# Kernel optimization log

Measured on AMD Instinct MI355X. Metric: run time of the kernel, lower is better.

## Reference

```python
import jax, jax.numpy as jnp
import numpy as np

E = 768   # embed_dim
N = 12    # num_heads
H = 128   # height
W = 128   # width
D = E // N  # head_dim = 64


def setup_inputs() -> dict:
    key = jax.random.key(0)
    ks = jax.random.split(key, 9)
    s = 0.02
    x = jax.random.normal(ks[0], (1, H * W, E), jnp.float32)
    Wq = jax.random.normal(ks[1], (E, E), jnp.float32) * s
    bq = jnp.zeros((E,), jnp.float32)
    Wk = jax.random.normal(ks[2], (E, E), jnp.float32) * s
    bk = jnp.zeros((E,), jnp.float32)
    Wv = jax.random.normal(ks[3], (E, E), jnp.float32) * s
    bv = jnp.zeros((E,), jnp.float32)
    Wo = jax.random.normal(ks[4], (E, E), jnp.float32) * s
    bo = jnp.zeros((E,), jnp.float32)
    return {"x": x, "Wq": Wq, "bq": bq, "Wk": Wk, "bk": bk,
            "Wv": Wv, "bv": bv, "Wo": Wo, "bo": bo}


def reference(x, Wq, bq, Wk, bk, Wv, bv, Wo, bo):
    # projections (torch Linear: x @ W.T + b)
    q = x @ Wq.T + bq
    k = x @ Wk.T + bk
    v = x @ Wv.T + bv

    # q, k -> (1, N, H, W, D)
    q = q.reshape(1, H, W, N, D).transpose(0, 3, 1, 2, 4)
    k = k.reshape(1, H, W, N, D).transpose(0, 3, 1, 2, 4)

    # --- width-axis attention (per row h) ---
    qr_w = q.transpose(0, 2, 1, 3, 4)  # (1, H, N, W, D)
    kr_w = k.transpose(0, 2, 1, 3, 4)  # (1, H, N, W, D)
    v = v.reshape(1, H, W, N, D).transpose(0, 1, 3, 2, 4)  # (1, H, N, W, D)
    # NOTE: original applies no 1/sqrt(D) scaling
    qk_w = jnp.einsum('bhnwd,bhnvd->bhnwv', qr_w, kr_w)  # (1, H, N, W, W)
    qk_w = jax.nn.softmax(qk_w, axis=-1)
    v = jnp.einsum('bhnwv,bhnvd->bhnwd', qk_w, v)  # (1, H, N, W, D)

    # --- height-axis attention (per column w) ---
    qr_h = q.transpose(0, 3, 1, 2, 4)  # (1, W, N, H, D)
    kr_h = k.transpose(0, 3, 1, 2, 4)  # (1, W, N, H, D)
    v = v.transpose(0, 3, 2, 1, 4)     # (1, W, N, H, D)
    qk_h = jnp.einsum('bwnhd,bwngd->bwnhg', qr_h, kr_h)  # (1, W, N, H, H)
    qk_h = jax.nn.softmax(qk_h, axis=-1)
    out = jnp.einsum('bwnhg,bwngd->bwnhd', qk_h, v)  # (1, W, N, H, D)

    # (1, W, N, H, D) -> (1, H, W, N, D) -> (1, H, W, E)
    out = out.transpose(0, 3, 1, 2, 4).reshape(1, H, W, E)
    out = out @ Wo.T + bo
    return out.reshape(1, H * W, E)
```

## Files before the change

kernel.cpp:

```cpp
#include <hip/hip_runtime.h>

typedef __attribute__((ext_vector_type(4))) float f32x4;
typedef __attribute__((ext_vector_type(8))) unsigned short u16x8;
typedef __attribute__((ext_vector_type(8))) __bf16 bf16x8;

typedef __attribute__((address_space(3))) unsigned lds_u32;
typedef const __attribute__((address_space(1))) unsigned glb_u32;

__device__ __forceinline__ unsigned short f2bf(float f) {
    union { float f; unsigned u; } v; v.f = f;
    unsigned r = v.u + 0x7fffu + ((v.u >> 16) & 1u);
    return (unsigned short)(r >> 16);
}

__device__ __forceinline__ f32x4 mfma16(u16x8 a, u16x8 b, f32x4 c) {
    return __builtin_amdgcn_mfma_f32_16x16x32_bf16(
        __builtin_bit_cast(bf16x8, a), __builtin_bit_cast(bf16x8, b), c, 0, 0, 0);
}

__device__ __forceinline__ void gload16(const unsigned short* g, unsigned short* l) {
    __builtin_amdgcn_global_load_lds((glb_u32*)g, (lds_u32*)l, 16, 0, 0);
}

#define BARM() asm volatile("s_barrier" ::: "memory")
#define WAITLGKM0() do { asm volatile("s_waitcnt lgkmcnt(0)" ::: "memory"); \
                         __builtin_amdgcn_sched_barrier(0); } while (0)
#define WAITVM6() asm volatile("s_waitcnt vmcnt(6)" ::: "memory")
#define WAITVM0() asm volatile("s_waitcnt vmcnt(0)" ::: "memory")

__global__ void cvt_f32_bf16(const float* __restrict__ src,
                             unsigned short* __restrict__ dst, int n) {
    int stride = gridDim.x * blockDim.x * 4;
    for (int i = (blockIdx.x * blockDim.x + threadIdx.x) * 4; i < n; i += stride) {
        float4 f = *reinterpret_cast<const float4*>(src + i);
        ushort4 o;
        o.x = f2bf(f.x); o.y = f2bf(f.y); o.z = f2bf(f.z); o.w = f2bf(f.w);
        *reinterpret_cast<ushort4*>(dst + i) = o;
    }
}

__global__ void cvt4_f32_bf16(const float* __restrict__ s0, const float* __restrict__ s1,
                              const float* __restrict__ s2, const float* __restrict__ s3,
                              unsigned short* __restrict__ dst, int per) {
    int total = per * 4;
    int stride = gridDim.x * blockDim.x * 4;
    for (int i = (blockIdx.x * blockDim.x + threadIdx.x) * 4; i < total; i += stride) {
        int w = i / per, off = i - w * per;
        const float* s = w == 0 ? s0 : w == 1 ? s1 : w == 2 ? s2 : s3;
        float4 f = *reinterpret_cast<const float4*>(s + off);
        ushort4 o;
        o.x = f2bf(f.x); o.y = f2bf(f.y); o.z = f2bf(f.z); o.w = f2bf(f.w);
        *reinterpret_cast<ushort4*>(dst + i) = o;
    }
}

template<bool OUTF32>
__global__ __launch_bounds__(512, 2) void gemm256(
    const unsigned short* __restrict__ A,
    const unsigned short* __restrict__ B,
    const float* __restrict__ b0, const float* __restrict__ b1, const float* __restrict__ b2,
    void* __restrict__ C0, void* __restrict__ C1, void* __restrict__ C2,
    int K, int NBY)
{
    __shared__ char lds[131072];
    const int t = threadIdx.x, lane = t & 63, wave = t >> 6;
    const int wm = wave >> 2, wn = wave & 3;

    const int nwg = gridDim.x;
    const int bid = blockIdx.x;
    const int swzb = (bid & 7) * (nwg >> 3) + (bid >> 3);
    const long m0 = (long)(swzb / NBY) * 256;
    const long n0 = (long)(swzb % NBY) * 256;

    const int NT = K >> 6;

    const int rloc = t >> 3;
    const int cel  = ((t & 7) ^ ((t >> 3) & 7)) << 3;
    const unsigned short* Abase = A + (m0 + rloc) * (long)K + cel;
    const unsigned short* Bbase = B + (n0 + rloc) * (long)K + cel;

    auto STAGEA = [&](int kt, int h) {
        char* dst = lds + ((kt & 1) << 15) + (h << 14) + (wave << 10);
        const unsigned short* src = Abase + (long)(h * 128) * K + kt * 64;
        gload16(src, (unsigned short*)dst);
        gload16(src + (long)64 * K, (unsigned short*)(dst + 8192));
    };
    auto STAGEB = [&](int kt, int h) {
        char* dst = lds + 65536 + ((kt & 1) << 15) + (h << 14) + (wave << 10);
        const unsigned short* src = Bbase + (long)(h * 128) * K + kt * 64;
        gload16(src, (unsigned short*)dst);
        gload16(src + (long)64 * K, (unsigned short*)(dst + 8192));
    };

    f32x4 acc[8][4] = {};
    u16x8 a[4][2], bl0[2][2], bl1[2][2];

    auto LDA8 = [&](int slot, int mh) {
        const char* buf = lds + (slot << 15) + (wm << 14);
        #pragma unroll
        for (int mi = 0; mi < 4; ++mi)
            #pragma unroll
            for (int kk = 0; kk < 2; ++kk) {
                int r = mh * 64 + mi * 16 + (lane & 15);
                int cb = kk * 64 + (lane >> 4) * 16;
                a[mi][kk] = *(const u16x8*)(buf + r * 128 + (cb ^ ((r & 7) << 4)));
            }
    };
    auto LDB4 = [&](int slot, int nh, u16x8 bf[2][2]) {
        const char* buf = lds + 65536 + (slot << 15) + ((wn >> 1) << 14);
        #pragma unroll
        for (int ni = 0; ni < 2; ++ni)
            #pragma unroll
            for (int kk = 0; kk < 2; ++kk) {
                int r = (wn & 1) * 64 + nh * 32 + ni * 16 + (lane & 15);
                int cb = kk * 64 + (lane >> 4) * 16;
                bf[ni][kk] = *(const u16x8*)(buf + r * 128 + (cb ^ ((r & 7) << 4)));
            }
    };
    auto MF16 = [&](int mh, int nh, u16x8 bf[2][2]) {
        __builtin_amdgcn_s_setprio(1);
        #pragma unroll
        for (int mi = 0; mi < 4; ++mi)
            #pragma unroll
            for (int ni = 0; ni < 2; ++ni)
                #pragma unroll
                for (int kk = 0; kk < 2; ++kk)
                    acc[mh * 4 + mi][nh * 2 + ni] =
                        mfma16(a[mi][kk], bf[ni][kk], acc[mh * 4 + mi][nh * 2 + ni]);
        __builtin_amdgcn_s_setprio(0);
    };

    STAGEA(0, 0); STAGEB(0, 0); STAGEB(0, 1); STAGEA(0, 1);
    STAGEA(1, 0); STAGEB(1, 0); STAGEB(1, 1);
    WAITVM0();
    BARM();

    for (int I = 0; I < (NT >> 1); ++I) {
        const int tb = 2 * I + 1;
        int t2 = 2 * I + 2; if (t2 >= NT) t2 -= 2;
        int t3 = 2 * I + 3; if (t3 >= NT) t3 -= 2;

        LDA8(0, 0); LDB4(0, 0, bl0); STAGEA(tb, 1);
        BARM(); WAITLGKM0();
        MF16(0, 0, bl0); BARM();
        LDB4(0, 1, bl1);
        BARM(); WAITLGKM0();
        MF16(0, 1, bl1); BARM();
        LDA8(0, 1); STAGEB(t2, 0);
        BARM(); WAITLGKM0();
        MF16(1, 1, bl1); BARM();
        STAGEA(t2, 0); STAGEB(t2, 1);
        WAITVM6(); BARM();
        MF16(1, 0, bl0); BARM();
        LDA8(1, 0); LDB4(1, 0, bl0); STAGEA(t2, 1);
        BARM(); WAITLGKM0();
        MF16(0, 0, bl0); BARM();
        LDB4(1, 1, bl1);
        BARM(); WAITLGKM0();
        MF16(0, 1, bl1); BARM();
        LDA8(1, 1); STAGEB(t3, 0);
        BARM(); WAITLGKM0();
        MF16(1, 1, bl1); BARM();
        STAGEA(t3, 0); STAGEB(t3, 1);
        WAITVM6(); BARM();
        MF16(1, 0, bl0); BARM();
    }

    #pragma unroll
    for (int mh = 0; mh < 2; ++mh)
        #pragma unroll
        for (int mi = 0; mi < 4; ++mi)
            #pragma unroll
            for (int nf = 0; nf < 4; ++nf) {
                int coln = (int)n0 + wn * 64 + nf * 16 + (lane & 15);
                int which = coln / 768;
                int nl = coln - which * 768;
                const float* bs = which == 0 ? b0 : (which == 1 ? b1 : b2);
                void* Cp       = which == 0 ? C0 : (which == 1 ? C1 : C2);
                float bias = bs[nl];
                #pragma unroll
                for (int q = 0; q < 4; ++q) {
                    long row = m0 + wm * 128 + mh * 64 + mi * 16 + ((lane >> 4) << 2) + q;
                    float val = acc[mh * 4 + mi][nf][q] + bias;
                    if (OUTF32) ((float*)Cp)[row * 768 + nl] = val;
                    else ((unsigned short*)Cp)[row * 768 + nl] = f2bf(val);
                }
            }
}

__global__ __launch_bounds__(256, 3) void attn128(
    const unsigned short* __restrict__ Q,
    const unsigned short* __restrict__ K,
    const unsigned short* __restrict__ V,
    unsigned short* __restrict__ O,
    int mult, int stride)
{
    __shared__ unsigned short QK[2][128][72];
    __shared__ unsigned short Vst[64][136];
    unsigned short (*Qs)[72] = QK[0];
    unsigned short (*Ks)[72] = QK[1];
    unsigned short (*Ps)[136] = (unsigned short (*)[136])&QK[0][0][0];

    const int pos = blockIdx.x, head = blockIdx.y;
    const int t = threadIdx.x, wave = t >> 6, lane = t & 63;

    for (int p = 0; p < 4; ++p) {
        int f = p * 2048 + t * 8;
        int r = f >> 6;
        int d = f & 63;
        long g = ((long)(pos * mult + r * stride)) * 768 + head * 64 + d;
        *(u16x8*)&Qs[r][d] = *(const u16x8*)&Q[g];
        *(u16x8*)&Ks[r][d] = *(const u16x8*)&K[g];
        u16x8 vv = *(const u16x8*)&V[g];
        #pragma unroll
        for (int j = 0; j < 8; ++j) Vst[d + j][r] = vv[j];
    }
    __syncthreads();

    const int rb = wave * 32;
    f32x4 s[2][8] = {};
    #pragma unroll
    for (int d0 = 0; d0 < 64; d0 += 32) {
        u16x8 a[2], b[8];
        #pragma unroll
        for (int mi = 0; mi < 2; ++mi)
            a[mi] = *(const u16x8*)&Qs[rb + mi * 16 + (lane & 15)][d0 + (lane >> 4) * 8];
        #pragma unroll
        for (int ni = 0; ni < 8; ++ni)
            b[ni] = *(const u16x8*)&Ks[ni * 16 + (lane & 15)][d0 + (lane >> 4) * 8];
        #pragma unroll
        for (int mi = 0; mi < 2; ++mi)
            #pragma unroll
            for (int ni = 0; ni < 8; ++ni)
                s[mi][ni] = mfma16(a[mi], b[ni], s[mi][ni]);
    }
    __syncthreads();

    #pragma unroll
    for (int mi = 0; mi < 2; ++mi) {
        #pragma unroll
        for (int q = 0; q < 4; ++q) {
            float m = -1e30f;
            #pragma unroll
            for (int ni = 0; ni < 8; ++ni) m = fmaxf(m, s[mi][ni][q]);
            m = fmaxf(m, __shfl_xor(m, 1));
            m = fmaxf(m, __shfl_xor(m, 2));
            m = fmaxf(m, __shfl_xor(m, 4));
            m = fmaxf(m, __shfl_xor(m, 8));
            float p[8], sum = 0.f;
            #pragma unroll
            for (int ni = 0; ni < 8; ++ni) { p[ni] = __expf(s[mi][ni][q] - m); sum += p[ni]; }
            sum += __shfl_xor(sum, 1);
            sum += __shfl_xor(sum, 2);
            sum += __shfl_xor(sum, 4);
            sum += __shfl_xor(sum, 8);
            float inv = 1.0f / sum;
            int row = rb + mi * 16 + ((lane >> 4) << 2) + q;
            #pragma unroll
            for (int ni = 0; ni < 8; ++ni)
                Ps[row][ni * 16 + (lane & 15)] = f2bf(p[ni] * inv);
        }
    }
    __syncthreads();

    f32x4 o[2][4] = {};
    #pragma unroll
    for (int v0 = 0; v0 < 128; v0 += 32) {
        u16x8 a[2], b[4];
        #pragma unroll
        for (int mi = 0; mi < 2; ++mi)
            a[mi] = *(const u16x8*)&Ps[rb + mi * 16 + (lane & 15)][v0 + (lane >> 4) * 8];
        #pragma unroll
        for (int ni = 0; ni < 4; ++ni)
            b[ni] = *(const u16x8*)&Vst[ni * 16 + (lane & 15)][v0 + (lane >> 4) * 8];
        #pragma unroll
        for (int mi = 0; mi < 2; ++mi)
            #pragma unroll
            for (int ni = 0; ni < 4; ++ni)
                o[mi][ni] = mfma16(a[mi], b[ni], o[mi][ni]);
    }

    #pragma unroll
    for (int mi = 0; mi < 2; ++mi)
        #pragma unroll
        for (int ni = 0; ni < 4; ++ni)
            #pragma unroll
            for (int q = 0; q < 4; ++q) {
                int row = rb + mi * 16 + ((lane >> 4) << 2) + q;
                int col = ni * 16 + (lane & 15);
                long g = ((long)(pos * mult + row * stride)) * 768 + head * 64 + col;
                O[g] = f2bf(o[mi][ni][q]);
            }
}

extern "C" void kernel_launch(void* const* d_in, const int* in_sizes, int n_in,
                              void* d_out, int out_size, void* d_ws, size_t ws_size,
                              hipStream_t stream) {
    const float* x  = (const float*)d_in[0];
    const float* Wq = (const float*)d_in[1];
    const float* bq = (const float*)d_in[2];
    const float* Wk = (const float*)d_in[3];
    const float* bk = (const float*)d_in[4];
    const float* Wv = (const float*)d_in[5];
    const float* bv = (const float*)d_in[6];
    const float* Wo = (const float*)d_in[7];
    const float* bo = (const float*)d_in[8];
    float* out = (float*)d_out;

    const size_t MS = (size_t)16384 * 768;
    const size_t WS = (size_t)768 * 768;
    unsigned short* xb   = (unsigned short*)d_ws;
    unsigned short* Qb   = xb + MS;
    unsigned short* Kb   = Qb + MS;
    unsigned short* Vb   = Kb + MS;
    unsigned short* Wqkv = Vb + MS;
    unsigned short* Wob  = Wqkv + 3 * WS;

    cvt_f32_bf16<<<2048, 256, 0, stream>>>(x, xb, (int)MS);
    cvt4_f32_bf16<<<2304, 256, 0, stream>>>(Wq, Wk, Wv, Wo, Wqkv, (int)WS);

    gemm256<false><<<576, 512, 0, stream>>>(
        xb, Wqkv, bq, bk, bv, Qb, Kb, Vb, 768, 9);

    attn128<<<dim3(128, 12), 256, 0, stream>>>(Qb, Kb, Vb, xb, 128, 1);
    attn128<<<dim3(128, 12), 256, 0, stream>>>(Qb, Kb, xb, Vb, 1, 128);

    gemm256<true><<<192, 512, 0, stream>>>(
        Vb, Wob, bo, bo, bo, out, out, out, 768, 3);
}
```

Baseline: 184.2 us.

## Reduce barriers and drop explicit LDS waits in GEMM main loop

```diff
diff --git a/kernel.cpp b/kernel.cpp
--- a/kernel.cpp
+++ b/kernel.cpp
@@ -23,8 +23,6 @@
 }
 
 #define BARM() asm volatile("s_barrier" ::: "memory")
-#define WAITLGKM0() do { asm volatile("s_waitcnt lgkmcnt(0)" ::: "memory"); \
-                         __builtin_amdgcn_sched_barrier(0); } while (0)
 #define WAITVM6() asm volatile("s_waitcnt vmcnt(6)" ::: "memory")
 #define WAITVM0() asm volatile("s_waitcnt vmcnt(0)" ::: "memory")
 
@@ -140,30 +138,38 @@
         int t2 = 2 * I + 2; if (t2 >= NT) t2 -= 2;
         int t3 = 2 * I + 3; if (t3 >= NT) t3 -= 2;
 
-        LDA8(0, 0); LDB4(0, 0, bl0); STAGEA(tb, 1);
-        BARM(); WAITLGKM0();
-        MF16(0, 0, bl0); BARM();
+        LDA8(0, 0); LDB4(0, 0, bl0);
+        BARM();
+        STAGEA(tb, 1);
+        MF16(0, 0, bl0);
         LDB4(0, 1, bl1);
-        BARM(); WAITLGKM0();
-        MF16(0, 1, bl1); BARM();
-        LDA8(0, 1); STAGEB(t2, 0);
-        BARM(); WAITLGKM0();
-        MF16(1, 1, bl1); BARM();
+        BARM();
+        MF16(0, 1, bl1);
+        LDA8(0, 1);
+        BARM();
+        STAGEB(t2, 0);
+        MF16(1, 1, bl1);
         STAGEA(t2, 0); STAGEB(t2, 1);
-        WAITVM6(); BARM();
-        MF16(1, 0, bl0); BARM();
-        LDA8(1, 0); LDB4(1, 0, bl0); STAGEA(t2, 1);
-        BARM(); WAITLGKM0();
-        MF16(0, 0, bl0); BARM();
+        WAITVM6();
+        BARM();
+        MF16(1, 0, bl0);
+        BARM();
+        LDA8(1, 0); LDB4(1, 0, bl0);
+        BARM();
+        STAGEA(t2, 1);
+        MF16(0, 0, bl0);
         LDB4(1, 1, bl1);
-        BARM(); WAITLGKM0();
-        MF16(0, 1, bl1); BARM();
-        LDA8(1, 1); STAGEB(t3, 0);
-        BARM(); WAITLGKM0();
-        MF16(1, 1, bl1); BARM();
+        BARM();
+        MF16(0, 1, bl1);
+        LDA8(1, 1);
+        BARM();
+        STAGEB(t3, 0);
+        MF16(1, 1, bl1);
         STAGEA(t3, 0); STAGEB(t3, 1);
-        WAITVM6(); BARM();
-        MF16(1, 0, bl0); BARM();
+        WAITVM6();
+        BARM();
+        MF16(1, 0, bl0);
+        BARM();
     }
 
     #pragma unroll
```

Result: no change. 180.7 us (-1.9%).
